# Performance work log

Measured on AMD Instinct MI355X. Metric: run time of the kernel, lower is better.

## Reference

```python
import jax, jax.numpy as jnp
import numpy as np

EPS = 1e-5


def setup_inputs() -> dict:
    key = jax.random.key(0)
    ks = jax.random.split(key, 12)
    B, S, M, D, H, dh = 8, 512, 512, 1024, 16, 64
    T = S + M
    w_scale = 0.03  # keep attention logits in a sane range (mimics nn.Linear init scale)
    return {
        "x": jax.random.normal(ks[0], (B, S, D), jnp.float32),
        "mem": jax.random.normal(ks[1], (B, M, D), jnp.float32),
        "R": jax.random.normal(ks[2], (T, D), jnp.float32),
        "u": jax.random.normal(ks[3], (1, H, 1, dh), jnp.float32) * 0.1,
        "t": jax.random.normal(ks[4], (1, H, 1, dh), jnp.float32) * 0.1,
        "Wq": jax.random.normal(ks[5], (H * dh, D), jnp.float32) * w_scale,
        "Wk": jax.random.normal(ks[6], (H * dh, D), jnp.float32) * w_scale,
        "Wv": jax.random.normal(ks[7], (H * dh, D), jnp.float32) * w_scale,
        "Wr": jax.random.normal(ks[8], (H * dh, D), jnp.float32) * w_scale,
        "Wo": jax.random.normal(ks[9], (D, H * dh), jnp.float32) * w_scale,
        "gamma": jnp.ones((D,), jnp.float32),
        "beta": jnp.zeros((D,), jnp.float32),
    }


def reference(x, mem, R, u, t, Wq, Wk, Wv, Wr, Wo, gamma, beta):
    B, S, D = x.shape
    H, dh = u.shape[1], u.shape[3]
    h = jnp.concatenate([mem, x], axis=1)          # [B, T, D]
    T = h.shape[1]
    M = T - S

    q = (x @ Wq.T).reshape(B, S, H, dh).transpose(0, 2, 1, 3)   # [B,H,S,dh]
    k = (h @ Wk.T).reshape(B, T, H, dh).transpose(0, 2, 1, 3)   # [B,H,T,dh]
    v = (h @ Wv.T).reshape(B, T, H, dh).transpose(0, 2, 1, 3)   # [B,H,T,dh]
    r = (R[-T:] @ Wr.T).reshape(1, T, H, dh).transpose(0, 2, 1, 3)  # [1,H,T,dh]

    ac = jnp.einsum("bhid,bhjd->bhij", q + u, k)                # [B,H,S,T]
    bd = jnp.einsum("bhid,hjd->bhij", q + t, r[0])              # [B,H,S,T]

    # circulant shift: shifted[..., i, j] = bd[..., i, (j - i + S - 1) % T]
    idx = (jnp.arange(T)[None, :] - jnp.arange(S)[:, None] + S - 1) % T  # [S,T]
    bd = jnp.take_along_axis(bd, idx[None, None], axis=3)

    # causal mask with memory offset: keep j <= i + M (tril(mem_len)), then
    # exact-zero entries (the masked ones) become -inf, matching the original.
    mask = jnp.arange(T)[None, :] <= (jnp.arange(S)[:, None] + M)        # [S,T]
    score = jnp.where(mask[None, None], (ac + bd) / jnp.sqrt(jnp.float32(dh)), 0.0)
    score = jnp.where(score == 0, -jnp.inf, score)
    p = jax.nn.softmax(score, axis=-1)                                   # [B,H,S,T]

    att = jnp.einsum("bhij,bhjd->bhid", p, v).transpose(0, 2, 1, 3).reshape(B, S, H * dh)
    out = att @ Wo.T                                                      # dropout is identity (p=0/eval)

    y = out + x
    mu = jnp.mean(y, axis=-1, keepdims=True)
    var = jnp.var(y, axis=-1, keepdims=True)
    return (y - mu) / jnp.sqrt(var + EPS) * gamma + beta
```

## Files before the change

kernel.cpp:

```cpp
#include <hip/hip_runtime.h>
#include <math.h>

#define BB 8
#define SS 512
#define MM 512
#define TT 1024
#define DD 1024
#define HH 16
#define DH 64

typedef __attribute__((ext_vector_type(8))) short bf16x8;
typedef __attribute__((ext_vector_type(4))) float f32x4;

#define SCL2E 0.1803368801111f
#define DTHR 11.5f

__device__ __forceinline__ ushort f2bf(float f) {
  union { float f; unsigned u; } x; x.f = f;
  unsigned r = x.u + 0x7fffu + ((x.u >> 16) & 1u);
  return (ushort)(r >> 16);
}
__device__ __forceinline__ float bf2f(ushort u) {
  return __builtin_bit_cast(float, ((unsigned)u) << 16);
}

__device__ __forceinline__ void stage16(void* lds, const void* g) {
  __builtin_amdgcn_global_load_lds((const __attribute__((address_space(1))) void*)g,
                                   (__attribute__((address_space(3))) void*)lds, 16, 0, 0);
}

template <int C>
__device__ __forceinline__ float dppf(float x) {
  return __builtin_bit_cast(float,
      __builtin_amdgcn_update_dpp(0, __builtin_bit_cast(int, x), C, 0xF, 0xF, true));
}
__device__ __forceinline__ float redmax16(float x) {
  x = fmaxf(x, dppf<0xB1>(x));
  x = fmaxf(x, dppf<0x4E>(x));
  x = fmaxf(x, dppf<0x141>(x));
  x = fmaxf(x, dppf<0x140>(x));
  return x;
}
__device__ __forceinline__ float redsum16(float x) {
  x += dppf<0xB1>(x);
  x += dppf<0x4E>(x);
  x += dppf<0x141>(x);
  x += dppf<0x140>(x);
  return x;
}
__device__ __forceinline__ float bperm_f(int byteaddr, float v) {
  return __builtin_bit_cast(float,
      __builtin_amdgcn_ds_bpermute(byteaddr, __builtin_bit_cast(int, v)));
}

__global__ __launch_bounds__(256) void cast_all(
    const float* __restrict__ mem, const float* __restrict__ x,
    const float* __restrict__ R, const float* __restrict__ Wq,
    const float* __restrict__ Wk, const float* __restrict__ Wv,
    const float* __restrict__ Wr, const float* __restrict__ Wo,
    ushort* __restrict__ hb, ushort* __restrict__ Rb, ushort* __restrict__ Wqb,
    ushort* __restrict__ Wkb, ushort* __restrict__ Wvb, ushort* __restrict__ Wrb,
    ushort* __restrict__ Wob) {
  const int M1 = 1 << 20;
  int i = (blockIdx.x * 256 + threadIdx.x) * 8;
  const float* src;
  ushort* dst;
  if (i < 4 * M1) {
    src = mem + i;
    dst = hb + (size_t)i + (size_t)(i >> 19) * 524288;
  } else if (i < 8 * M1) {
    int j = i - 4 * M1;
    src = x + j;
    dst = hb + (size_t)j + (size_t)(j >> 19) * 524288 + 524288;
  } else if (i < 9 * M1) {
    src = R + (i - 8 * M1);  dst = Rb + (i - 8 * M1);
  } else if (i < 10 * M1) {
    src = Wq + (i - 9 * M1); dst = Wqb + (i - 9 * M1);
  } else if (i < 11 * M1) {
    src = Wk + (i - 10 * M1); dst = Wkb + (i - 10 * M1);
  } else if (i < 12 * M1) {
    src = Wv + (i - 11 * M1); dst = Wvb + (i - 11 * M1);
  } else if (i < 13 * M1) {
    src = Wr + (i - 12 * M1); dst = Wrb + (i - 12 * M1);
  } else {
    src = Wo + (i - 13 * M1); dst = Wob + (i - 13 * M1);
  }
  float4 a = *(const float4*)(src);
  float4 c = *(const float4*)(src + 4);
  union { bf16x8 v; ushort u[8]; } pk;
  pk.u[0] = f2bf(a.x); pk.u[1] = f2bf(a.y); pk.u[2] = f2bf(a.z); pk.u[3] = f2bf(a.w);
  pk.u[4] = f2bf(c.x); pk.u[5] = f2bf(c.y); pk.u[6] = f2bf(c.z); pk.u[7] = f2bf(c.w);
  *(bf16x8*)(void*)dst = pk.v;
}

__global__ __launch_bounds__(256) void gemm_qkvr(
    const ushort* __restrict__ hb, const ushort* __restrict__ Rbuf,
    const ushort* __restrict__ Wqb, const ushort* __restrict__ Wkb,
    const ushort* __restrict__ Wvb, const ushort* __restrict__ Wrb,
    ushort* __restrict__ qub,
    ushort* __restrict__ kbo, ushort* __restrict__ vtb, ushort* __restrict__ rbo,
    const float* __restrict__ uvec) {
  __shared__ ushort As[128 * 32];
  __shared__ ushort Bs[128 * 32];
  const int bid = (blockIdx.x & 7) * 168 + (blockIdx.x >> 3);
  const ushort* A;
  const ushort* W;
  ushort* C0 = nullptr;
  bool qadd = false, qslice = false, vmode = false;
  int mt, nx;
  if (bid < 256) {
    int r = bid; mt = r >> 3; nx = r & 7;
    A = hb; W = Wqb; C0 = qub; qadd = true; qslice = true;
  } else if (bid < 768) {
    int r = bid - 256; mt = r >> 3; nx = r & 7;
    A = hb; W = Wkb; C0 = kbo;
  } else if (bid < 1280) {
    int r = bid - 768; mt = r >> 3; nx = r & 7;
    A = hb; W = Wvb; C0 = vtb; vmode = true;
  } else {
    int r = bid - 1280; mt = r >> 3; nx = r & 7;
    A = Rbuf; W = Wrb; C0 = rbo;
  }
  const int m0 = mt * 128, n0 = nx * 128;

  const int t = threadIdx.x;
  const int w = t >> 6, l = t & 63;
  const int m16 = l & 15, kg = l >> 4;
  const int wr = w >> 1, wc = w & 1;

  const int c0 = t, c1 = t + 256;
  const int scol = (((t & 3) ^ ((t >> 3) & 3)) * 8);
  const ushort* asrc0;
  const ushort* asrc1;
  {
    int gm0 = m0 + (c0 >> 2), gm1 = m0 + (c1 >> 2);
    if (qslice) {
      asrc0 = A + ((size_t)((gm0 >> 9) * TT + MM + (gm0 & 511))) * DD + scol;
      asrc1 = A + ((size_t)((gm1 >> 9) * TT + MM + (gm1 & 511))) * DD + scol;
    } else {
      asrc0 = A + (size_t)gm0 * DD + scol;
      asrc1 = A + (size_t)gm1 * DD + scol;
    }
  }
  const ushort* bsrc0 = W + (size_t)(n0 + (c0 >> 2)) * DD + scol;
  const ushort* bsrc1 = W + (size_t)(n0 + (c1 >> 2)) * DD + scol;
  ushort* adst0 = As + c0 * 8;
  ushort* adst1 = As + c1 * 8;
  ushort* bdst0 = Bs + c0 * 8;
  ushort* bdst1 = Bs + c1 * 8;

  const int cbx = ((kg ^ ((m16 >> 1) & 3)) << 3);

  f32x4 acc[4][4];
#pragma unroll
  for (int mi = 0; mi < 4; ++mi)
#pragma unroll
    for (int ni = 0; ni < 4; ++ni) acc[mi][ni] = (f32x4){0.f, 0.f, 0.f, 0.f};

  for (int k0 = 0; k0 < DD; k0 += 32) {
    stage16(adst0, asrc0 + k0);
    stage16(adst1, asrc1 + k0);
    stage16(bdst0, bsrc0 + k0);
    stage16(bdst1, bsrc1 + k0);
    __syncthreads();
    bf16x8 af[4], bfr[4];
#pragma unroll
    for (int mi = 0; mi < 4; ++mi)
      af[mi] = *(const bf16x8*)(const void*)&As[(wr * 64 + mi * 16 + m16) * 32 + cbx];
#pragma unroll
    for (int ni = 0; ni < 4; ++ni)
      bfr[ni] = *(const bf16x8*)(const void*)&Bs[(wc * 64 + ni * 16 + m16) * 32 + cbx];
#pragma unroll
    for (int mi = 0; mi < 4; ++mi)
#pragma unroll
      for (int ni = 0; ni < 4; ++ni)
        acc[mi][ni] = __builtin_amdgcn_mfma_f32_16x16x32_bf16(af[mi], bfr[ni], acc[mi][ni], 0, 0, 0);
    __syncthreads();
  }

  const int rbase = m0 + wr * 64 + kg * 4;
  const int cbase = n0 + wc * 64 + m16;
  if (vmode) {
    const int bb = m0 >> 10;
    const int tt0 = (m0 & 1023) + wr * 64 + kg * 4;
#pragma unroll
    for (int mi = 0; mi < 4; ++mi)
#pragma unroll
      for (int ni = 0; ni < 4; ++ni) {
        ushort4 o;
        o.x = f2bf(acc[mi][ni][0]); o.y = f2bf(acc[mi][ni][1]);
        o.z = f2bf(acc[mi][ni][2]); o.w = f2bf(acc[mi][ni][3]);
        *(ushort4*)(C0 + ((size_t)(bb * 1024 + cbase + ni * 16) << 10) + tt0 + mi * 16) = o;
      }
  } else if (qadd) {
    float uv[4];
#pragma unroll
    for (int ni = 0; ni < 4; ++ni) uv[ni] = uvec[cbase + ni * 16];
#pragma unroll
    for (int mi = 0; mi < 4; ++mi)
#pragma unroll
      for (int ni = 0; ni < 4; ++ni)
#pragma unroll
        for (int rg = 0; rg < 4; ++rg)
          C0[(size_t)(rbase + mi * 16 + rg) * DD + cbase + ni * 16] = f2bf(acc[mi][ni][rg] + uv[ni]);
  } else {
#pragma unroll
    for (int mi = 0; mi < 4; ++mi)
#pragma unroll
      for (int ni = 0; ni < 4; ++ni)
#pragma unroll
        for (int rg = 0; rg < 4; ++rg)
          C0[(size_t)(rbase + mi * 16 + rg) * DD + cbase + ni * 16] = f2bf(acc[mi][ni][rg]);
  }
}

__global__ __launch_bounds__(256) void gemm_wo(const ushort* __restrict__ A,
                                               const ushort* __restrict__ W,
                                               ushort* __restrict__ Cb) {
  __shared__ ushort As[128 * 32];
  __shared__ ushort Bs[64 * 32];
  const int bid = (blockIdx.x & 7) * 64 + (blockIdx.x >> 3);
  const int mt = bid >> 4, nxt = bid & 15;
  const int m0 = mt * 128, n0 = nxt * 64;
  const int t = threadIdx.x;
  const int w = t >> 6, l = t & 63;
  const int m16 = l & 15, kg = l >> 4;
  const int wr = w >> 1, wc = w & 1;

  const int scol = (((t & 3) ^ ((t >> 3) & 3)) * 8);
  const ushort* asrc0 = A + (size_t)(m0 + (t >> 2)) * DD + scol;
  const ushort* asrc1 = A + (size_t)(m0 + 64 + (t >> 2)) * DD + scol;
  const ushort* bsrc0 = W + (size_t)(n0 + (t >> 2)) * DD + scol;
  ushort* adst0 = As + t * 8;
  ushort* adst1 = As + (t + 256) * 8;
  ushort* bdst0 = Bs + t * 8;

  const int cbx = ((kg ^ ((m16 >> 1) & 3)) << 3);

  f32x4 acc[4][2];
#pragma unroll
  for (int mi = 0; mi < 4; ++mi)
#pragma unroll
    for (int ni = 0; ni < 2; ++ni) acc[mi][ni] = (f32x4){0.f, 0.f, 0.f, 0.f};

  for (int k0 = 0; k0 < DD; k0 += 32) {
    stage16(adst0, asrc0 + k0);
    stage16(adst1, asrc1 + k0);
    stage16(bdst0, bsrc0 + k0);
    __syncthreads();
    bf16x8 af[4], bfr[2];
#pragma unroll
    for (int mi = 0; mi < 4; ++mi)
      af[mi] = *(const bf16x8*)(const void*)&As[(wr * 64 + mi * 16 + m16) * 32 + cbx];
#pragma unroll
    for (int ni = 0; ni < 2; ++ni)
      bfr[ni] = *(const bf16x8*)(const void*)&Bs[(wc * 32 + ni * 16 + m16) * 32 + cbx];
#pragma unroll
    for (int mi = 0; mi < 4; ++mi)
#pragma unroll
      for (int ni = 0; ni < 2; ++ni)
        acc[mi][ni] = __builtin_amdgcn_mfma_f32_16x16x32_bf16(af[mi], bfr[ni], acc[mi][ni], 0, 0, 0);
    __syncthreads();
  }

  const int rbase = m0 + wr * 64 + kg * 4;
  const int cbase = n0 + wc * 32 + m16;
#pragma unroll
  for (int mi = 0; mi < 4; ++mi)
#pragma unroll
    for (int ni = 0; ni < 2; ++ni)
#pragma unroll
      for (int rg = 0; rg < 4; ++rg)
        Cb[(size_t)(rbase + mi * 16 + rg) * DD + cbase + ni * 16] = f2bf(acc[mi][ni][rg]);
}

__global__ __launch_bounds__(256) void attn_mfma(const ushort* __restrict__ qu,
                                                 const ushort* __restrict__ kb,
                                                 const ushort* __restrict__ vt,
                                                 const ushort* __restrict__ rb,
                                                 const float* __restrict__ uvec,
                                                 const float* __restrict__ tvec,
                                                 ushort* __restrict__ att) {
  const int w = threadIdx.x >> 6;
  const int l = threadIdx.x & 63;
  const int m16 = l & 15;
  const int kg = l >> 4;
  const int bid = blockIdx.x;
  const int it = 7 - (bid >> 7);
  const int bh = bid & 127;
  const int b = bh >> 4, h = bh & 15;
  const int i0 = it * 64;

  __shared__ ushort Ks[2][4096];
  __shared__ ushort Vs[4096];
  __shared__ ushort Rl[8192];
  __shared__ ushort plds[4][16][72];

  bf16x8 aqu[2], aqt[2];
  {
    const ushort* qrow = qu + ((size_t)(b * SS + i0 + w * 16 + m16)) * DD + h * DH + kg * 8;
    aqu[0] = *(const bf16x8*)(const void*)(qrow);
    aqu[1] = *(const bf16x8*)(const void*)(qrow + 32);
#pragma unroll
    for (int ks = 0; ks < 2; ++ks) {
      ushort* a = (ushort*)&aqt[ks];
      const ushort* qa = (const ushort*)&aqu[ks];
#pragma unroll
      for (int e = 0; e < 8; ++e) {
        const int col = h * DH + kg * 8 + ks * 32 + e;
        a[e] = f2bf(bf2f(qa[e]) + (tvec[col] - uvec[col]));
      }
    }
  }

  int baddr[4];
  bool bsel[4];
#pragma unroll
  for (int rg = 0; rg < 4; ++rg) {
    const int rw = kg * 4 + rg;
    baddr[rg] = (kg * 16 + ((m16 + 15 - rw) & 15)) << 2;
    bsel[rg] = m16 > rw;
  }

  const int c0 = threadIdx.x, c1 = threadIdx.x + 256;
  const int r0 = c0 >> 3, sc0 = ((c0 & 7) * 8) ^ ((r0 & 7) << 3);
  const int r1 = c1 >> 3, sc1 = ((c1 & 7) * 8) ^ ((r1 & 7) << 3);
  const ushort* kp0 = kb + ((size_t)(b * TT) + r0) * DD + h * DH + sc0;
  const ushort* kp1 = kb + ((size_t)(b * TT) + r1) * DD + h * DH + sc1;
  const ushort* vp0 = vt + ((size_t)(b * 1024 + h * DH + r0)) * 1024 + sc0;
  const ushort* vp1 = vt + ((size_t)(b * 1024 + h * DH + r1)) * 1024 + sc1;

  const int cb0 = (kg * 8) ^ ((m16 & 7) << 3);
  const int cb1 = (kg * 8 + 32) ^ ((m16 & 7) << 3);
  int slot64[5];
#pragma unroll
  for (int f = 0; f < 5; ++f)
    slot64[f] = ((496 - i0 - w * 16 + m16 + f * 16) & 127) << 6;

  {
    const int base0 = 448 - i0;
#pragma unroll
    for (int kk = 0; kk < 4; ++kk) {
      int c = threadIdx.x + kk * 256;
      int ro = c >> 3, cc = c & 7;
      int p = base0 + ro;
      int slot = p & 127;
      stage16(Rl + slot * 64 + cc * 8,
              rb + (size_t)p * DD + h * DH + ((cc * 8) ^ ((ro & 7) << 3)));
    }
  }
  stage16(&Ks[0][c0 * 8], kp0);
  stage16(&Ks[0][c1 * 8], kp1);
  stage16(Vs + c0 * 8, vp0);
  stage16(Vs + c1 * 8, vp1);
  kp0 += (size_t)64 * DD; kp1 += (size_t)64 * DD;
  vp0 += 64; vp1 += 64;

  f32x4 O[4];
  float mrow[4], lrow[4];
#pragma unroll
  for (int nt = 0; nt < 4; ++nt) O[nt] = (f32x4){0.f, 0.f, 0.f, 0.f};
#pragma unroll
  for (int rg = 0; rg < 4; ++rg) { mrow[rg] = -1e30f; lrow[rg] = 0.f; }

  const int ntj = it + 9;
  int cur = 0;
  for (int jt = 0; jt < ntj; ++jt) {
    const int j0 = jt * 64;

    if (jt > 0) {
      stage16(Vs + c0 * 8, vp0);
      stage16(Vs + c1 * 8, vp1);
      vp0 += 64; vp1 += 64;
      const int pstart = 512 + j0 - i0;
#pragma unroll
      for (int kk = 0; kk < 2; ++kk) {
        int c = threadIdx.x + kk * 256;
        int ro = c >> 3, cc = c & 7;
        int p = pstart + ro;
        int pc = p < 1023 ? p : 1023;
        int slot = p & 127;
        stage16(Rl + slot * 64 + cc * 8,
                rb + (size_t)pc * DD + h * DH + ((cc * 8) ^ ((ro & 7) << 3)));
      }
    }
    __syncthreads();

    const ushort* kbase = &Ks[cur][0];
    f32x4 ac[4];
    __builtin_amdgcn_s_setprio(1);
#pragma unroll
    for (int nt = 0; nt < 4; ++nt) {
      ac[nt] = (f32x4){0.f, 0.f, 0.f, 0.f};
      const int row = nt * 16 + m16;
#pragma unroll
      for (int ks = 0; ks < 2; ++ks) {
        bf16x8 bk = *(const bf16x8*)(const void*)(kbase + row * 64 + (ks == 0 ? cb0 : cb1));
        ac[nt] = __builtin_amdgcn_mfma_f32_16x16x32_bf16(aqu[ks], bk, ac[nt], 0, 0, 0);
      }
    }
    __builtin_amdgcn_s_setprio(0);

    if (jt + 1 < ntj) {
      stage16(&Ks[cur ^ 1][c0 * 8], kp0);
      stage16(&Ks[cur ^ 1][c1 * 8], kp1);
      kp0 += (size_t)64 * DD; kp1 += (size_t)64 * DD;
    }

    f32x4 bd[5];
    __builtin_amdgcn_s_setprio(1);
#pragma unroll
    for (int f = 0; f < 5; ++f) {
      f32x4 z = (f32x4){0.f, 0.f, 0.f, 0.f};
      bf16x8 b0 = *(const bf16x8*)(const void*)(Rl + slot64[f] + cb0);
      z = __builtin_amdgcn_mfma_f32_16x16x32_bf16(aqt[0], b0, z, 0, 0, 0);
      bf16x8 b1 = *(const bf16x8*)(const void*)(Rl + slot64[f] + cb1);
      bd[f] = __builtin_amdgcn_mfma_f32_16x16x32_bf16(aqt[1], b1, z, 0, 0, 0);
    }
    __builtin_amdgcn_s_setprio(0);
#pragma unroll
    for (int f = 0; f < 5; ++f) slot64[f] = (slot64[f] + 4096) & 8191;

    float sca[4][4];
#pragma unroll
    for (int rg = 0; rg < 4; ++rg) {
      float rr[5];
#pragma unroll
      for (int f = 0; f < 5; ++f) rr[f] = bperm_f(baddr[rg], bd[f][rg]);
#pragma unroll
      for (int nt = 0; nt < 4; ++nt) {
        float bdv = bsel[rg] ? rr[nt + 1] : rr[nt];
        sca[nt][rg] = (ac[nt][rg] + bdv) * SCL2E;
      }
    }
    if (jt == ntj - 1) {
#pragma unroll
      for (int rg = 0; rg < 4; ++rg) {
        const int jmax = i0 + w * 16 + kg * 4 + rg + MM;
#pragma unroll
        for (int nt = 0; nt < 4; ++nt)
          sca[nt][rg] = (j0 + nt * 16 + m16 <= jmax) ? sca[nt][rg] : -1e30f;
      }
    }

    float pmax[4];
#pragma unroll
    for (int rg = 0; rg < 4; ++rg) {
      float pm = fmaxf(fmaxf(sca[0][rg], sca[1][rg]), fmaxf(sca[2][rg], sca[3][rg]));
      pmax[rg] = redmax16(pm);
    }
    bool grow = false;
#pragma unroll
    for (int rg = 0; rg < 4; ++rg) grow = grow || (pmax[rg] > mrow[rg] + DTHR);
    if (__any(grow)) {
#pragma unroll
      for (int rg = 0; rg < 4; ++rg) {
        float mnew = fmaxf(mrow[rg], pmax[rg]);
        float scale = __builtin_amdgcn_exp2f(mrow[rg] - mnew);
        mrow[rg] = mnew;
        lrow[rg] *= scale;
#pragma unroll
        for (int nt = 0; nt < 4; ++nt) O[nt][rg] *= scale;
      }
    }

#pragma unroll
    for (int rg = 0; rg < 4; ++rg) {
      float ps = 0.f;
#pragma unroll
      for (int nt = 0; nt < 4; ++nt) {
        float p = __builtin_amdgcn_exp2f(sca[nt][rg] - mrow[rg]);
        ps += p;
        plds[w][kg * 4 + rg][nt * 16 + m16] = f2bf(p);
      }
      lrow[rg] += redsum16(ps);
    }

    __builtin_amdgcn_s_setprio(1);
#pragma unroll
    for (int ks = 0; ks < 2; ++ks) {
      bf16x8 pa = *(const bf16x8*)(const void*)&plds[w][m16][kg * 8 + ks * 32];
#pragma unroll
      for (int nt = 0; nt < 4; ++nt) {
        bf16x8 vf = *(const bf16x8*)(const void*)(Vs + (nt * 16 + m16) * 64 + (ks == 0 ? cb0 : cb1));
        O[nt] = __builtin_amdgcn_mfma_f32_16x16x32_bf16(pa, vf, O[nt], 0, 0, 0);
      }
    }
    __builtin_amdgcn_s_setprio(0);

    __syncthreads();
    cur ^= 1;
  }

  float linv[4];
#pragma unroll
  for (int rg = 0; rg < 4; ++rg) linv[rg] = 1.f / lrow[rg];
#pragma unroll
  for (int nt = 0; nt < 4; ++nt) {
#pragma unroll
    for (int rg = 0; rg < 4; ++rg) {
      att[((size_t)(b * SS + i0 + w * 16 + kg * 4 + rg)) * DD + h * DH + nt * 16 + m16] =
          f2bf(O[nt][rg] * linv[rg]);
    }
  }
}

__global__ __launch_bounds__(256) void ln_kernel(const ushort* __restrict__ ypre,
                                                 const ushort* __restrict__ hb,
                                                 const float* __restrict__ gamma,
                                                 const float* __restrict__ beta,
                                                 float* __restrict__ out) {
  const int row = blockIdx.x;
  const int t = threadIdx.x;
  const int lane = t & 63, w = t >> 6;
  const ushort* yr = ypre + (size_t)row * DD;
  const ushort* xr = hb + ((size_t)((row >> 9) * TT + MM + (row & 511))) * DD;

  ushort4 yv = *(const ushort4*)(yr + t * 4);
  ushort4 xv = *(const ushort4*)(xr + t * 4);
  float v0 = bf2f(yv.x) + bf2f(xv.x), v1 = bf2f(yv.y) + bf2f(xv.y);
  float v2 = bf2f(yv.z) + bf2f(xv.z), v3 = bf2f(yv.w) + bf2f(xv.w);

  float s = v0 + v1 + v2 + v3;
  float ss = v0 * v0 + v1 * v1 + v2 * v2 + v3 * v3;
  __shared__ float rs[4], rss[4];
#pragma unroll
  for (int off = 32; off; off >>= 1) {
    s += __shfl_xor(s, off);
    ss += __shfl_xor(ss, off);
  }
  if (!lane) { rs[w] = s; rss[w] = ss; }
  __syncthreads();
  s = rs[0] + rs[1] + rs[2] + rs[3];
  ss = rss[0] + rss[1] + rss[2] + rss[3];
  const float mu = s * (1.f / DD);
  const float var = ss * (1.f / DD) - mu * mu;
  const float rstd = rsqrtf(var + 1e-5f);

  float4 g = *(const float4*)(gamma + t * 4);
  float4 be = *(const float4*)(beta + t * 4);
  float4 o;
  o.x = (v0 - mu) * rstd * g.x + be.x;
  o.y = (v1 - mu) * rstd * g.y + be.y;
  o.z = (v2 - mu) * rstd * g.z + be.z;
  o.w = (v3 - mu) * rstd * g.w + be.w;
  *(float4*)(out + (size_t)row * DD + t * 4) = o;
}

extern "C" void kernel_launch(void* const* d_in, const int* in_sizes, int n_in,
                              void* d_out, int out_size, void* d_ws, size_t ws_size,
                              hipStream_t stream) {
  const float* x = (const float*)d_in[0];
  const float* mem = (const float*)d_in[1];
  const float* R = (const float*)d_in[2];
  const float* u = (const float*)d_in[3];
  const float* tv = (const float*)d_in[4];
  const float* Wq = (const float*)d_in[5];
  const float* Wk = (const float*)d_in[6];
  const float* Wv = (const float*)d_in[7];
  const float* Wr = (const float*)d_in[8];
  const float* Wo = (const float*)d_in[9];
  const float* gamma = (const float*)d_in[10];
  const float* beta = (const float*)d_in[11];
  float* out = (float*)d_out;

  ushort* hb = (ushort*)d_ws;
  ushort* Rb = hb + (8u << 20);
  ushort* Wqb = Rb + (1u << 20);
  ushort* Wkb = Wqb + (1u << 20);
  ushort* Wvb = Wkb + (1u << 20);
  ushort* Wrb = Wvb + (1u << 20);
  ushort* Wob = Wrb + (1u << 20);
  ushort* qu_b = Wob + (1u << 20);
  ushort* kb = qu_b + (4u << 20);
  ushort* vt = kb + (8u << 20);
  ushort* rb = vt + (8u << 20);
  ushort* att = qu_b;
  ushort* ypre = kb;

  dim3 blk(256);

  cast_all<<<dim3(7168), blk, 0, stream>>>(mem, x, R, Wq, Wk, Wv, Wr, Wo,
                                           hb, Rb, Wqb, Wkb, Wvb, Wrb, Wob);

  gemm_qkvr<<<dim3(1344), blk, 0, stream>>>(hb, Rb, Wqb, Wkb, Wvb, Wrb,
                                            qu_b, kb, vt, rb, u);

  attn_mfma<<<dim3(BB * HH * 8), blk, 0, stream>>>(qu_b, kb, vt, rb, u, tv, att);

  gemm_wo<<<dim3(512), blk, 0, stream>>>(att, Wob, ypre);

  ln_kernel<<<dim3(BB * SS), blk, 0, stream>>>(ypre, hb, gamma, beta, out);
}
```

Before: 172.4 us.

## Double-buffer LDS staging in projection GEMMs and interleave K/V tiles

Both projection GEMMs now use two LDS buffers and prefetch the next K-slice while MFMAs run on the current one. Synchronisation moves to raw s_barrier plus explicit vmcnt waits, which assumes stage16 issues direct-to-LDS loads counted by vmcnt. The QKVR kernel also interleaves the K and V tiles for the same rows so that neighbouring blocks share the A tile in cache. The trade-offs are doubled LDS use, which may lower occupancy, and reliance on hand-written wait counts being correct.

```diff
diff --git a/kernel.cpp b/kernel.cpp
--- a/kernel.cpp
+++ b/kernel.cpp
@@ -100,8 +100,8 @@
     ushort* __restrict__ qub,
     ushort* __restrict__ kbo, ushort* __restrict__ vtb, ushort* __restrict__ rbo,
     const float* __restrict__ uvec) {
-  __shared__ ushort As[128 * 32];
-  __shared__ ushort Bs[128 * 32];
+  __shared__ ushort As[2][4096];
+  __shared__ ushort Bs[2][4096];
   const int bid = (blockIdx.x & 7) * 168 + (blockIdx.x >> 3);
   const ushort* A;
   const ushort* W;
@@ -109,16 +109,17 @@
   bool qadd = false, qslice = false, vmode = false;
   int mt, nx;
   if (bid < 256) {
-    int r = bid; mt = r >> 3; nx = r & 7;
+    mt = bid >> 3; nx = bid & 7;
     A = hb; W = Wqb; C0 = qub; qadd = true; qslice = true;
-  } else if (bid < 768) {
-    int r = bid - 256; mt = r >> 3; nx = r & 7;
-    A = hb; W = Wkb; C0 = kbo;
   } else if (bid < 1280) {
-    int r = bid - 768; mt = r >> 3; nx = r & 7;
-    A = hb; W = Wvb; C0 = vtb; vmode = true;
+    int r2 = bid - 256;
+    mt = r2 >> 4;
+    int sub = r2 & 15;
+    nx = sub & 7;
+    if (sub < 8) { A = hb; W = Wkb; C0 = kbo; }
+    else { A = hb; W = Wvb; C0 = vtb; vmode = true; }
   } else {
-    int r = bid - 1280; mt = r >> 3; nx = r & 7;
+    int r2 = bid - 1280; mt = r2 >> 3; nx = r2 & 7;
     A = Rbuf; W = Wrb; C0 = rbo;
   }
   const int m0 = mt * 128, n0 = nx * 128;
@@ -144,10 +145,6 @@
   }
   const ushort* bsrc0 = W + (size_t)(n0 + (c0 >> 2)) * DD + scol;
   const ushort* bsrc1 = W + (size_t)(n0 + (c1 >> 2)) * DD + scol;
-  ushort* adst0 = As + c0 * 8;
-  ushort* adst1 = As + c1 * 8;
-  ushort* bdst0 = Bs + c0 * 8;
-  ushort* bdst1 = Bs + c1 * 8;
 
   const int cbx = ((kg ^ ((m16 >> 1) & 3)) << 3);
 
@@ -157,25 +154,38 @@
 #pragma unroll
     for (int ni = 0; ni < 4; ++ni) acc[mi][ni] = (f32x4){0.f, 0.f, 0.f, 0.f};
 
-  for (int k0 = 0; k0 < DD; k0 += 32) {
-    stage16(adst0, asrc0 + k0);
-    stage16(adst1, asrc1 + k0);
-    stage16(bdst0, bsrc0 + k0);
-    stage16(bdst1, bsrc1 + k0);
-    __syncthreads();
+  stage16(&As[0][c0 * 8], asrc0);
+  stage16(&As[0][c1 * 8], asrc1);
+  stage16(&Bs[0][c0 * 8], bsrc0);
+  stage16(&Bs[0][c1 * 8], bsrc1);
+
+  for (int kt = 0; kt < 32; ++kt) {
+    const int bf = kt & 1;
+    asm volatile("s_barrier" ::: "memory");
+    if (kt < 31) {
+      const int k1 = (kt + 1) << 5;
+      stage16(&As[bf ^ 1][c0 * 8], asrc0 + k1);
+      stage16(&As[bf ^ 1][c1 * 8], asrc1 + k1);
+      stage16(&Bs[bf ^ 1][c0 * 8], bsrc0 + k1);
+      stage16(&Bs[bf ^ 1][c1 * 8], bsrc1 + k1);
+      asm volatile("s_waitcnt vmcnt(4)" ::: "memory");
+    } else {
+      asm volatile("s_waitcnt vmcnt(0)" ::: "memory");
+    }
+    asm volatile("s_barrier" ::: "memory");
+
     bf16x8 af[4], bfr[4];
 #pragma unroll
     for (int mi = 0; mi < 4; ++mi)
-      af[mi] = *(const bf16x8*)(const void*)&As[(wr * 64 + mi * 16 + m16) * 32 + cbx];
+      af[mi] = *(const bf16x8*)(const void*)&As[bf][(wr * 64 + mi * 16 + m16) * 32 + cbx];
 #pragma unroll
     for (int ni = 0; ni < 4; ++ni)
-      bfr[ni] = *(const bf16x8*)(const void*)&Bs[(wc * 64 + ni * 16 + m16) * 32 + cbx];
+      bfr[ni] = *(const bf16x8*)(const void*)&Bs[bf][(wc * 64 + ni * 16 + m16) * 32 + cbx];
 #pragma unroll
     for (int mi = 0; mi < 4; ++mi)
 #pragma unroll
       for (int ni = 0; ni < 4; ++ni)
         acc[mi][ni] = __builtin_amdgcn_mfma_f32_16x16x32_bf16(af[mi], bfr[ni], acc[mi][ni], 0, 0, 0);
-    __syncthreads();
   }
 
   const int rbase = m0 + wr * 64 + kg * 4;
@@ -217,8 +227,8 @@
 __global__ __launch_bounds__(256) void gemm_wo(const ushort* __restrict__ A,
                                                const ushort* __restrict__ W,
                                                ushort* __restrict__ Cb) {
-  __shared__ ushort As[128 * 32];
-  __shared__ ushort Bs[64 * 32];
+  __shared__ ushort As[2][4096];
+  __shared__ ushort Bs[2][2048];
   const int bid = (blockIdx.x & 7) * 64 + (blockIdx.x >> 3);
   const int mt = bid >> 4, nxt = bid & 15;
   const int m0 = mt * 128, n0 = nxt * 64;
@@ -231,9 +241,6 @@
   const ushort* asrc0 = A + (size_t)(m0 + (t >> 2)) * DD + scol;
   const ushort* asrc1 = A + (size_t)(m0 + 64 + (t >> 2)) * DD + scol;
   const ushort* bsrc0 = W + (size_t)(n0 + (t >> 2)) * DD + scol;
-  ushort* adst0 = As + t * 8;
-  ushort* adst1 = As + (t + 256) * 8;
-  ushort* bdst0 = Bs + t * 8;
 
   const int cbx = ((kg ^ ((m16 >> 1) & 3)) << 3);
 
@@ -243,24 +250,35 @@
 #pragma unroll
     for (int ni = 0; ni < 2; ++ni) acc[mi][ni] = (f32x4){0.f, 0.f, 0.f, 0.f};
 
-  for (int k0 = 0; k0 < DD; k0 += 32) {
-    stage16(adst0, asrc0 + k0);
-    stage16(adst1, asrc1 + k0);
-    stage16(bdst0, bsrc0 + k0);
-    __syncthreads();
+  stage16(&As[0][t * 8], asrc0);
+  stage16(&As[0][(t + 256) * 8], asrc1);
+  if (t < 256) stage16(&Bs[0][t * 8], bsrc0);
+  for (int kt = 0; kt < 32; ++kt) {
+    const int bf = kt & 1;
+    asm volatile("s_barrier" ::: "memory");
+    if (kt < 31) {
+      const int k1 = (kt + 1) << 5;
+      stage16(&As[bf ^ 1][t * 8], asrc0 + k1);
+      stage16(&As[bf ^ 1][(t + 256) * 8], asrc1 + k1);
+      stage16(&Bs[bf ^ 1][t * 8], bsrc0 + k1);
+      asm volatile("s_waitcnt vmcnt(3)" ::: "memory");
+    } else {
+      asm volatile("s_waitcnt vmcnt(0)" ::: "memory");
+    }
+    asm volatile("s_barrier" ::: "memory");
+
     bf16x8 af[4], bfr[2];
 #pragma unroll
     for (int mi = 0; mi < 4; ++mi)
-      af[mi] = *(const bf16x8*)(const void*)&As[(wr * 64 + mi * 16 + m16) * 32 + cbx];
+      af[mi] = *(const bf16x8*)(const void*)&As[bf][(wr * 64 + mi * 16 + m16) * 32 + cbx];
 #pragma unroll
     for (int ni = 0; ni < 2; ++ni)
-      bfr[ni] = *(const bf16x8*)(const void*)&Bs[(wc * 32 + ni * 16 + m16) * 32 + cbx];
+      bfr[ni] = *(const bf16x8*)(const void*)&Bs[bf][(wc * 32 + ni * 16 + m16) * 32 + cbx];
 #pragma unroll
     for (int mi = 0; mi < 4; ++mi)
 #pragma unroll
       for (int ni = 0; ni < 2; ++ni)
         acc[mi][ni] = __builtin_amdgcn_mfma_f32_16x16x32_bf16(af[mi], bfr[ni], acc[mi][ni], 0, 0, 0);
-    __syncthreads();
   }
 
   const int rbase = m0 + wr * 64 + kg * 4;
```

New measurement: 181.2 us. 1.05x slower.

## Double-buffer LDS tiles in QKVR GEMM with async global-to-LDS prefetch

Applied to the files above, without the earlier changes.

Splits the shared-memory A/B tiles of the QKVR projection GEMM into two buffers and prefetches the next K-slice while MFMA compute runs on the current one. Explicit vmcnt waits and s_barrier calls replace the two __syncthreads per iteration, and launch bounds request four blocks per CU. This is meant to hide global-load latency behind compute. It doubles LDS per block, which may limit occupancy, and it depends on stage16 being an async LDS load counted by vmcnt.

```diff
diff --git a/kernel.cpp b/kernel.cpp
--- a/kernel.cpp
+++ b/kernel.cpp
@@ -93,15 +93,14 @@
   *(bf16x8*)(void*)dst = pk.v;
 }
 
-__global__ __launch_bounds__(256) void gemm_qkvr(
+__global__ __launch_bounds__(256, 4) void gemm_qkvr(
     const ushort* __restrict__ hb, const ushort* __restrict__ Rbuf,
     const ushort* __restrict__ Wqb, const ushort* __restrict__ Wkb,
     const ushort* __restrict__ Wvb, const ushort* __restrict__ Wrb,
     ushort* __restrict__ qub,
     ushort* __restrict__ kbo, ushort* __restrict__ vtb, ushort* __restrict__ rbo,
     const float* __restrict__ uvec) {
-  __shared__ ushort As[128 * 32];
-  __shared__ ushort Bs[128 * 32];
+  __shared__ ushort As0[4096], Bs0[4096], As1[4096], Bs1[4096];
   const int bid = (blockIdx.x & 7) * 168 + (blockIdx.x >> 3);
   const ushort* A;
   const ushort* W;
@@ -109,7 +108,7 @@
   bool qadd = false, qslice = false, vmode = false;
   int mt, nx;
   if (bid < 256) {
-    int r = bid; mt = r >> 3; nx = r & 7;
+    mt = bid >> 3; nx = bid & 7;
     A = hb; W = Wqb; C0 = qub; qadd = true; qslice = true;
   } else if (bid < 768) {
     int r = bid - 256; mt = r >> 3; nx = r & 7;
@@ -144,12 +143,10 @@
   }
   const ushort* bsrc0 = W + (size_t)(n0 + (c0 >> 2)) * DD + scol;
   const ushort* bsrc1 = W + (size_t)(n0 + (c1 >> 2)) * DD + scol;
-  ushort* adst0 = As + c0 * 8;
-  ushort* adst1 = As + c1 * 8;
-  ushort* bdst0 = Bs + c0 * 8;
-  ushort* bdst1 = Bs + c1 * 8;
 
   const int cbx = ((kg ^ ((m16 >> 1) & 3)) << 3);
+  const int arow0 = (wr * 64 + m16) * 32 + cbx;
+  const int brow0 = (wc * 64 + m16) * 32 + cbx;
 
   f32x4 acc[4][4];
 #pragma unroll
@@ -157,26 +154,48 @@
 #pragma unroll
     for (int ni = 0; ni < 4; ++ni) acc[mi][ni] = (f32x4){0.f, 0.f, 0.f, 0.f};
 
-  for (int k0 = 0; k0 < DD; k0 += 32) {
-    stage16(adst0, asrc0 + k0);
-    stage16(adst1, asrc1 + k0);
-    stage16(bdst0, bsrc0 + k0);
-    stage16(bdst1, bsrc1 + k0);
-    __syncthreads();
-    bf16x8 af[4], bfr[4];
-#pragma unroll
-    for (int mi = 0; mi < 4; ++mi)
-      af[mi] = *(const bf16x8*)(const void*)&As[(wr * 64 + mi * 16 + m16) * 32 + cbx];
-#pragma unroll
-    for (int ni = 0; ni < 4; ++ni)
-      bfr[ni] = *(const bf16x8*)(const void*)&Bs[(wc * 64 + ni * 16 + m16) * 32 + cbx];
-#pragma unroll
-    for (int mi = 0; mi < 4; ++mi)
-#pragma unroll
-      for (int ni = 0; ni < 4; ++ni)
-        acc[mi][ni] = __builtin_amdgcn_mfma_f32_16x16x32_bf16(af[mi], bfr[ni], acc[mi][ni], 0, 0, 0);
-    __syncthreads();
-  }
+#define QKVR_STAGE(AS, BS, KOFF)                \
+  do {                                          \
+    stage16(AS + c0 * 8, asrc0 + (KOFF));       \
+    stage16(AS + c1 * 8, asrc1 + (KOFF));       \
+    stage16(BS + c0 * 8, bsrc0 + (KOFF));       \
+    stage16(BS + c1 * 8, bsrc1 + (KOFF));       \
+  } while (0)
+
+#define QKVR_COMPUTE(AS, BS)                                                      \
+  do {                                                                            \
+    bf16x8 af[4], bfr[4];                                                         \
+    _Pragma("unroll") for (int mi = 0; mi < 4; ++mi)                              \
+        af[mi] = *(const bf16x8*)(const void*)&AS[arow0 + mi * 512];              \
+    _Pragma("unroll") for (int ni = 0; ni < 4; ++ni)                              \
+        bfr[ni] = *(const bf16x8*)(const void*)&BS[brow0 + ni * 512];             \
+    _Pragma("unroll") for (int mi = 0; mi < 4; ++mi)                              \
+        _Pragma("unroll") for (int ni = 0; ni < 4; ++ni)                          \
+            acc[mi][ni] = __builtin_amdgcn_mfma_f32_16x16x32_bf16(                \
+                af[mi], bfr[ni], acc[mi][ni], 0, 0, 0);                           \
+  } while (0)
+
+  QKVR_STAGE(As0, Bs0, 0);
+
+#pragma unroll 1
+  for (int kt = 0; kt < 32; kt += 2) {
+    QKVR_STAGE(As1, Bs1, (kt + 1) << 5);
+    asm volatile("s_waitcnt vmcnt(4)" ::: "memory");
+    __builtin_amdgcn_s_barrier();
+    QKVR_COMPUTE(As0, Bs0);
+    __builtin_amdgcn_s_barrier();
+    if (kt + 2 < 32) {
+      QKVR_STAGE(As0, Bs0, (kt + 2) << 5);
+      asm volatile("s_waitcnt vmcnt(4)" ::: "memory");
+    } else {
+      asm volatile("s_waitcnt vmcnt(0)" ::: "memory");
+    }
+    __builtin_amdgcn_s_barrier();
+    QKVR_COMPUTE(As1, Bs1);
+    __builtin_amdgcn_s_barrier();
+  }
+#undef QKVR_STAGE
+#undef QKVR_COMPUTE
 
   const int rbase = m0 + wr * 64 + kg * 4;
   const int cbase = n0 + wc * 64 + m16;
```

Result: faster. 162.2 us (-6.0%).
